# Performance work log

Measured on AMD Instinct MI355X. Metric: run time of the kernel, lower is better.

Reference implementation:

```python
import jax, jax.numpy as jnp
import numpy as np

B, NQ, NUM_CLASSES, K = 64, 300, 80, 150
NC = 4 + NUM_CLASSES  # channels per query
POOL = 32             # 640 -> 20 spatial via 32x32 mean pooling (surrogate backbone)


def setup_inputs() -> dict:
    key = jax.random.key(0)
    k1, k2 = jax.random.split(key)
    x = jax.random.randint(k1, (B, 3, 640, 640), 0, 256, dtype=jnp.int32)  # uint8-like image
    W = jax.random.normal(k2, (3 * 20 * 20, NQ * NC), dtype=jnp.float32) * 0.02
    return {"x": x, "W": W}


def reference(x, W):
    # --- preprocessing (faithful to original) ---
    xf = x.astype(jnp.float32) / 255.0
    xf = xf[:, jnp.array([2, 1, 0]), :, :]  # BGR -> RGB

    # --- opaque backbone surrogate: avg-pool 640->20, flatten, linear ---
    b, c, h, w = xf.shape
    pooled = xf.reshape(b, c, h // POOL, POOL, w // POOL, POOL).mean(axis=(3, 5))  # [B,3,20,20]
    y = (pooled.reshape(b, -1) @ W).reshape(-1, NQ, NC)  # [B,300,84]

    # --- postprocessing chain (the kernel target) ---
    boxes = y[:, :, :4]           # [B,300,4]
    class_scores = y[:, :, 4:]    # [B,300,80]
    max_scores = class_scores.max(axis=2)      # [B,300]
    class_ids = class_scores.argmax(axis=2)    # [B,300] (first-index ties, same as torch.max)
    topk_scores, topk_idx = jax.lax.top_k(max_scores, K)  # sorted descending, as torch.topk(sorted=True)
    topk_boxes = jnp.take_along_axis(boxes, topk_idx[:, :, None], axis=1)  # [B,K,4]
    topk_ids = jnp.take_along_axis(class_ids, topk_idx, axis=1)            # [B,K]
    return jnp.concatenate(
        [topk_boxes, topk_scores[:, :, None], topk_ids[:, :, None].astype(jnp.float32)],
        axis=2,
    )  # [B,K,6]
```

## Files before the change

kernel.cpp:

```cpp
#include <hip/hip_runtime.h>
#include <stdint.h>

#define BATCH 64
#define NQ 300
#define NCLS 80
#define NCH 84
#define KTOP 150
#define NTOT (NQ * NCH)
#define KDIM 1200
#define HW 640

#define WS_Y   614400
#define WS_SC  13516800
#define WS_CID 13670400

__global__ __launch_bounds__(256) void pool_kernel(const int* __restrict__ x,
                                                   double* __restrict__ At) {
  int wave = threadIdx.x >> 6;
  int lane = threadIdx.x & 63;
  int cell = blockIdx.x * 4 + wave;
  int b   = cell / 1200;
  int rem = cell - b * 1200;
  int cin = rem / 400;
  int pp  = rem - cin * 400;
  int ph = pp / 20, pw = pp - ph * 20;
  const int* base = x + (((b * 3 + cin) * HW) + ph * 32) * HW + pw * 32;
  int r  = lane >> 1;
  int c0 = (lane & 1) * 16;
  const int4* p = (const int4*)(base + r * HW + c0);
  int4 v0 = p[0], v1 = p[1], v2 = p[2], v3 = p[3];
  int s = v0.x + v0.y + v0.z + v0.w + v1.x + v1.y + v1.z + v1.w
        + v2.x + v2.y + v2.z + v2.w + v3.x + v3.y + v3.z + v3.w;
  #pragma unroll
  for (int off = 32; off > 0; off >>= 1) s += __shfl_down(s, off);
  if (lane == 0) {
    int kout = (2 - cin) * 400 + pp;
    At[kout * 64 + b] = (double)s * (1.0 / 261120.0);
  }
}

__global__ __launch_bounds__(256) void gemm_kernel(const double* __restrict__ At,
                                                   const float* __restrict__ W,
                                                   double* __restrict__ Y) {
  int wave = threadIdx.x >> 6;
  int lane = threadIdx.x & 63;
  int row0 = __builtin_amdgcn_readfirstlane((int)(blockIdx.y * 32 + wave * 8));
  int n  = blockIdx.x * 64 + lane;
  int nl = n < NTOT ? n : NTOT - 1;
  const double* Ap = At + row0;
  const float*  Wp = W + nl;
  double acc[8];
  #pragma unroll
  for (int i = 0; i < 8; ++i) acc[i] = 0.0;
  float w[8];
  #pragma unroll
  for (int u = 0; u < 8; ++u) w[u] = Wp[(size_t)u * NTOT];
  #pragma unroll 1
  for (int k0 = 0; k0 < KDIM; k0 += 8) {
    int kn = (k0 + 8 == KDIM) ? 0 : k0 + 8;
    float wn[8];
    #pragma unroll
    for (int u = 0; u < 8; ++u) wn[u] = Wp[(size_t)(kn + u) * NTOT];
    #pragma unroll
    for (int u = 0; u < 8; ++u) {
      double wd = (double)w[u];
      #pragma unroll
      for (int i = 0; i < 8; ++i)
        acc[i] = fma(Ap[(size_t)(k0 + u) * 64 + i], wd, acc[i]);
    }
    #pragma unroll
    for (int u = 0; u < 8; ++u) w[u] = wn[u];
  }
  if (n < NTOT) {
    #pragma unroll
    for (int i = 0; i < 8; ++i)
      Y[(size_t)(row0 + i) * NTOT + n] = acc[i];
  }
}

__global__ __launch_bounds__(256) void argmax_kernel(const double* __restrict__ Y,
                                                     double* __restrict__ sc,
                                                     int* __restrict__ cid) {
  int wave = threadIdx.x >> 6;
  int lane = threadIdx.x & 63;
  int task = blockIdx.x * 4 + wave;
  int b = task / NQ;
  int q = task - b * NQ;
  const double* y = Y + (size_t)b * NTOT + q * NCH;
  double best = y[4 + lane];
  int    cls  = lane;
  if (lane < 16) {
    double v2 = y[68 + lane];
    if (v2 > best) { best = v2; cls = 64 + lane; }
  }
  #pragma unroll
  for (int off = 32; off > 0; off >>= 1) {
    double ob = __shfl_down(best, off);
    int    oc = __shfl_down(cls, off);
    if (ob > best || (ob == best && oc < cls)) { best = ob; cls = oc; }
  }
  if (lane == 0) { sc[task] = best; cid[task] = cls; }
}

__global__ __launch_bounds__(256) void select_kernel(const double* __restrict__ Y,
                                                     const double* __restrict__ sc,
                                                     const int* __restrict__ cid,
                                                     float* __restrict__ out) {
  __shared__ double ssc[NQ];
  __shared__ int    scid[NQ];
  int b = blockIdx.x;
  int t = threadIdx.x;
  for (int q = t; q < NQ; q += 256) {
    ssc[q]  = sc[b * NQ + q];
    scid[q] = cid[b * NQ + q];
  }
  __syncthreads();
  for (int q = t; q < NQ; q += 256) {
    double s = ssc[q];
    int rank = 0;
    for (int j = 0; j < NQ; ++j) {
      double sj = ssc[j];
      rank += (sj > s) || (sj == s && j < q);
    }
    if (rank < KTOP) {
      const double* row = Y + (size_t)b * NTOT + q * NCH;
      float* o = out + ((size_t)b * KTOP + rank) * 6;
      o[0] = (float)row[0];
      o[1] = (float)row[1];
      o[2] = (float)row[2];
      o[3] = (float)row[3];
      o[4] = (float)s;
      o[5] = (float)scid[q];
    }
  }
}

extern "C" void kernel_launch(void* const* d_in, const int* in_sizes, int n_in,
                              void* d_out, int out_size, void* d_ws, size_t ws_size,
                              hipStream_t stream) {
  const int*   x = (const int*)d_in[0];
  const float* W = (const float*)d_in[1];
  double* At  = (double*)d_ws;
  double* Y   = (double*)((char*)d_ws + WS_Y);
  double* sc  = (double*)((char*)d_ws + WS_SC);
  int*    cid = (int*)((char*)d_ws + WS_CID);
  pool_kernel<<<dim3(19200), dim3(256), 0, stream>>>(x, At);
  gemm_kernel<<<dim3(394, 2), dim3(256), 0, stream>>>(At, W, Y);
  argmax_kernel<<<dim3(4800), dim3(256), 0, stream>>>(Y, sc, cid);
  select_kernel<<<dim3(64), dim3(256), 0, stream>>>(Y, sc, cid, (float*)d_out);
}
```

Baseline: 614.6 us.

## Split GEMM K dimension into two chunks and reduce partials downstream

The GEMM's reduction dimension is split into two halves processed by separate blocks, doubling the grid to raise occupancy and shorten each block's serial loop. Each half writes its own partial output buffer, and the argmax and select kernels sum the two partials when reading. This adds an extra partial-output buffer write and read traffic in exchange for more parallelism.

After: 591.3 us. 1.04x faster.

```diff
diff --git a/kernel.cpp b/kernel.cpp
--- a/kernel.cpp
+++ b/kernel.cpp
@@ -8,11 +8,12 @@
 #define KTOP 150
 #define NTOT (NQ * NCH)
 #define KDIM 1200
+#define KCH  600
 #define HW 640
 
 #define WS_Y   614400
-#define WS_SC  13516800
-#define WS_CID 13670400
+#define WS_SC  26419200
+#define WS_CID 26572800
 
 __global__ __launch_bounds__(256) void pool_kernel(const int* __restrict__ x,
                                                    double* __restrict__ At) {
@@ -42,13 +43,15 @@
 __global__ __launch_bounds__(256) void gemm_kernel(const double* __restrict__ At,
                                                    const float* __restrict__ W,
                                                    double* __restrict__ Y) {
-  int wave = threadIdx.x >> 6;
-  int lane = threadIdx.x & 63;
-  int row0 = __builtin_amdgcn_readfirstlane((int)(blockIdx.y * 32 + wave * 8));
+  int wave  = threadIdx.x >> 6;
+  int lane  = threadIdx.x & 63;
+  int grp   = blockIdx.y & 1;
+  int chunk = blockIdx.y >> 1;
+  int row0 = __builtin_amdgcn_readfirstlane((int)(grp * 32 + wave * 8));
   int n  = blockIdx.x * 64 + lane;
   int nl = n < NTOT ? n : NTOT - 1;
-  const double* Ap = At + row0;
-  const float*  Wp = W + nl;
+  const double* Ap = At + (size_t)chunk * KCH * 64 + row0;
+  const float*  Wp = W + (size_t)chunk * KCH * NTOT + nl;
   double acc[8];
   #pragma unroll
   for (int i = 0; i < 8; ++i) acc[i] = 0.0;
@@ -56,8 +59,8 @@
   #pragma unroll
   for (int u = 0; u < 8; ++u) w[u] = Wp[(size_t)u * NTOT];
   #pragma unroll 1
-  for (int k0 = 0; k0 < KDIM; k0 += 8) {
-    int kn = (k0 + 8 == KDIM) ? 0 : k0 + 8;
+  for (int k0 = 0; k0 < KCH; k0 += 8) {
+    int kn = (k0 + 8 == KCH) ? 0 : k0 + 8;
     float wn[8];
     #pragma unroll
     for (int u = 0; u < 8; ++u) wn[u] = Wp[(size_t)(kn + u) * NTOT];
@@ -72,9 +75,9 @@
     for (int u = 0; u < 8; ++u) w[u] = wn[u];
   }
   if (n < NTOT) {
+    double* Yp = Y + ((size_t)chunk * BATCH + row0) * NTOT + n;
     #pragma unroll
-    for (int i = 0; i < 8; ++i)
-      Y[(size_t)(row0 + i) * NTOT + n] = acc[i];
+    for (int i = 0; i < 8; ++i) Yp[(size_t)i * NTOT] = acc[i];
   }
 }
 
@@ -86,11 +89,12 @@
   int task = blockIdx.x * 4 + wave;
   int b = task / NQ;
   int q = task - b * NQ;
-  const double* y = Y + (size_t)b * NTOT + q * NCH;
-  double best = y[4 + lane];
+  const double* y0 = Y + (size_t)b * NTOT + q * NCH;
+  const double* y1 = y0 + (size_t)BATCH * NTOT;
+  double best = y0[4 + lane] + y1[4 + lane];
   int    cls  = lane;
   if (lane < 16) {
-    double v2 = y[68 + lane];
+    double v2 = y0[68 + lane] + y1[68 + lane];
     if (v2 > best) { best = v2; cls = 64 + lane; }
   }
   #pragma unroll
@@ -123,12 +127,13 @@
       rank += (sj > s) || (sj == s && j < q);
     }
     if (rank < KTOP) {
-      const double* row = Y + (size_t)b * NTOT + q * NCH;
+      const double* r0 = Y + (size_t)b * NTOT + q * NCH;
+      const double* r1 = r0 + (size_t)BATCH * NTOT;
       float* o = out + ((size_t)b * KTOP + rank) * 6;
-      o[0] = (float)row[0];
-      o[1] = (float)row[1];
-      o[2] = (float)row[2];
-      o[3] = (float)row[3];
+      o[0] = (float)(r0[0] + r1[0]);
+      o[1] = (float)(r0[1] + r1[1]);
+      o[2] = (float)(r0[2] + r1[2]);
+      o[3] = (float)(r0[3] + r1[3]);
       o[4] = (float)s;
       o[5] = (float)scid[q];
     }
@@ -145,7 +150,7 @@
   double* sc  = (double*)((char*)d_ws + WS_SC);
   int*    cid = (int*)((char*)d_ws + WS_CID);
   pool_kernel<<<dim3(19200), dim3(256), 0, stream>>>(x, At);
-  gemm_kernel<<<dim3(394, 2), dim3(256), 0, stream>>>(At, W, Y);
+  gemm_kernel<<<dim3(394, 4), dim3(256), 0, stream>>>(At, W, Y);
   argmax_kernel<<<dim3(4800), dim3(256), 0, stream>>>(Y, sc, cid);
   select_kernel<<<dim3(64), dim3(256), 0, stream>>>(Y, sc, cid, (float*)d_out);
 }
```
